# Performance work log

Measured on AMD Instinct MI355X. Metric: run time of the kernel, lower is better.

Reference implementation:

```python
import jax, jax.numpy as jnp
import numpy as np

D_MODEL = 1024
N_HEADS = 16
HEAD_DIM = D_MODEL // N_HEADS


def setup_inputs() -> dict:
    key = jax.random.key(0)
    k1, k2, k3 = jax.random.split(key, 3)
    x = jax.random.normal(k1, (4, 2048, D_MODEL), dtype=jnp.float32)
    # torch Linear(d, 3d, bias=False): y = x @ W.T with W [3d, d]; store transposed [d, 3d]
    s = 1.0 / np.sqrt(D_MODEL)
    w_qkv = jax.random.uniform(k2, (D_MODEL, 3 * D_MODEL), dtype=jnp.float32, minval=-s, maxval=s)
    w_proj = jax.random.uniform(k3, (D_MODEL, D_MODEL), dtype=jnp.float32, minval=-s, maxval=s)
    return {"x": x, "w_qkv": w_qkv, "w_proj": w_proj}


def reference(x, w_qkv, w_proj):
    B, T, D = x.shape
    qkv = (x @ w_qkv).reshape(B, T, 3, N_HEADS, HEAD_DIM)
    qkv = jnp.transpose(qkv, (2, 0, 3, 1, 4))  # [3, B, H, T, hd]
    q, k, v = qkv[0], qkv[1], qkv[2]
    # NOTE: original module applies NO 1/sqrt(head_dim) scaling
    attn = jax.nn.softmax(jnp.einsum('bhqd,bhkd->bhqk', q, k), axis=-1)
    out = jnp.einsum('bhqk,bhkd->bhqd', attn, v)
    out = jnp.transpose(out, (0, 2, 1, 3)).reshape(B, T, D)
    return out @ w_proj
```

## Files before the change

### kernel.cpp

```cpp
#include <hip/hip_runtime.h>

typedef __bf16 bf16;
typedef __bf16 bf16x8 __attribute__((ext_vector_type(8)));
typedef float f32x4 __attribute__((ext_vector_type(4)));
typedef unsigned int uint;
typedef unsigned short ushort;

typedef const __attribute__((address_space(1))) void* gas_ptr;
typedef __attribute__((address_space(3))) void* las_ptr;

__device__ __forceinline__ void load16_lds(const void* g, void* l) {
  __builtin_amdgcn_global_load_lds((gas_ptr)g, (las_ptr)l, 16, 0, 0);
}

__global__ __launch_bounds__(256) void cast_f32_bf16(
    const float* __restrict__ in, bf16* __restrict__ out) {
  size_t i = (size_t)blockIdx.x * 256 + threadIdx.x;
  const float4* p = reinterpret_cast<const float4*>(in) + i * 2;
  float4 a = p[0], b = p[1];
  bf16x8 v;
  v[0] = (bf16)a.x; v[1] = (bf16)a.y; v[2] = (bf16)a.z; v[3] = (bf16)a.w;
  v[4] = (bf16)b.x; v[5] = (bf16)b.y; v[6] = (bf16)b.z; v[7] = (bf16)b.w;
  reinterpret_cast<bf16x8*>(out)[i] = v;
}

__global__ __launch_bounds__(256) void transpose_f32_bf16(
    const float* __restrict__ in, bf16* __restrict__ out, int K, int N) {
  __shared__ __attribute__((aligned(16))) bf16 tile[64 * 72];
  const int k0 = blockIdx.y * 64, n0 = blockIdx.x * 64;
  const int tid = threadIdx.x;
  for (int c = tid; c < 1024; c += 256) {
    int ki = c >> 4, j4 = c & 15;
    float4 f = *reinterpret_cast<const float4*>(in + (size_t)(k0 + ki) * N + n0 + j4 * 4);
    bf16* t = &tile[ki * 72 + j4 * 4];
    t[0] = (bf16)f.x; t[1] = (bf16)f.y; t[2] = (bf16)f.z; t[3] = (bf16)f.w;
  }
  __syncthreads();
  for (int c = tid; c < 512; c += 256) {
    int ni = c >> 3, k8 = c & 7;
    bf16x8 v;
    for (int j = 0; j < 8; j++) v[j] = tile[(k8 * 8 + j) * 72 + ni];
    *reinterpret_cast<bf16x8*>(out + (size_t)(n0 + ni) * K + k0 + k8 * 8) = v;
  }
}

template <typename CT>
__global__ __launch_bounds__(256, 2) void gemm_lds(
    const bf16* __restrict__ A, const bf16* __restrict__ Bt,
    CT* __restrict__ C, int M, int N, int K) {
  __shared__ __attribute__((aligned(16))) bf16 As[128 * 64];
  __shared__ __attribute__((aligned(16))) bf16 Bs[128 * 64];
  const int tid = threadIdx.x;
  const int wave = tid >> 6;
  const int lane = tid & 63;
  const int l15 = lane & 15;
  const int quad = lane >> 4;
  const int nwg = gridDim.x * gridDim.y;
  const int orig = blockIdx.y * gridDim.x + blockIdx.x;
  const int swz = (orig & 7) * (nwg >> 3) + (orig >> 3);
  const int m0 = (swz / gridDim.x) * 128;
  const int n0 = (swz % gridDim.x) * 128;
  const int wm = (wave >> 1) * 64;
  const int wn = (wave & 1) * 64;

  f32x4 acc[4][4] = {};

  for (int kt = 0; kt < K; kt += 64) {
    __syncthreads();
    for (int it = 0; it < 4; ++it) {
      int p = it * 256 + wave * 64 + lane;
      int row = p >> 3, kc = (p & 7) ^ (row & 7);
      load16_lds(A + (size_t)(m0 + row) * K + kt + kc * 8, &As[p * 8]);
      load16_lds(Bt + (size_t)(n0 + row) * K + kt + kc * 8, &Bs[p * 8]);
    }
    __syncthreads();
    for (int kk = 0; kk < 64; kk += 32) {
      const int kc = (kk >> 3) + quad;
      bf16x8 af[4], bfr[4];
      for (int i = 0; i < 4; i++) {
        int row = wm + i * 16 + l15;
        af[i] = *reinterpret_cast<const bf16x8*>(&As[(row * 8 + (kc ^ (row & 7))) * 8]);
      }
      for (int j = 0; j < 4; j++) {
        int row = wn + j * 16 + l15;
        bfr[j] = *reinterpret_cast<const bf16x8*>(&Bs[(row * 8 + (kc ^ (row & 7))) * 8]);
      }
      for (int i = 0; i < 4; i++)
        for (int j = 0; j < 4; j++)
          acc[i][j] = __builtin_amdgcn_mfma_f32_16x16x32_bf16(af[i], bfr[j], acc[i][j], 0, 0, 0);
    }
  }

  for (int i = 0; i < 4; i++)
    for (int j = 0; j < 4; j++)
      for (int r = 0; r < 4; r++) {
        int row = m0 + wm + i * 16 + quad * 4 + r;
        int col = n0 + wn + j * 16 + l15;
        C[(size_t)row * N + col] = (CT)acc[i][j][r];
      }
}

__device__ __forceinline__ int vs_dw(int d, int kdw) {
  return d * 32 + (kdw ^ ((((d >> 3) ^ d) & 7) * 4));
}

__global__ __launch_bounds__(512, 4) void attn_kernel(
    const bf16* __restrict__ qkv, bf16* __restrict__ out) {
  __shared__ __attribute__((aligned(16))) bf16 Ks[2][64 * 64];
  __shared__ __attribute__((aligned(16))) uint Vs[2][64 * 32];

  const int tid = threadIdx.x;
  const int wave = tid >> 6;
  const int lane = tid & 63;
  const int l15 = lane & 15;
  const int quad = lane >> 4;
  const int b = blockIdx.x >> 4;
  const int h = blockIdx.x & 15;
  const int qt0 = blockIdx.y * 128;
  const bf16* base = qkv + (size_t)b * 2048 * 3072 + h * 64;
  const float L2E = 1.44269504f;

  bf16x8 aq0, aq1;
  {
    const bf16* qrow = base + (size_t)(qt0 + wave * 16 + l15) * 3072;
    aq0 = *reinterpret_cast<const bf16x8*>(qrow + quad * 8);
    aq1 = *reinterpret_cast<const bf16x8*>(qrow + 32 + quad * 8);
    for (int j = 0; j < 8; j++) {
      aq0[j] = (bf16)((float)aq0[j] * L2E);
      aq1[j] = (bf16)((float)aq1[j] * L2E);
    }
  }

  bf16x8 bones = {};
  if (l15 == 0)
    for (int j = 0; j < 8; j++) bones[j] = (bf16)1.0f;

  f32x4 nm = {};
  f32x4 o[4] = {};
  f32x4 l_acc = {};

  const int t2 = tid & 255;
  const int kp = t2 >> 3;
  const int oct = t2 & 7;
  const bool vrole = (wave < 4);
  const int prow = ((kp & 4) << 2) | ((kp & 24) >> 1) | (kp & 3);
  const int kxor = oct ^ (prow & 7);
  const int kdst0 = (prow * 8 + kxor) * 8;
  const int kdst1 = kdst0 + 32 * 64;

  bf16x8 pre0, pre1;
  if (vrole) {
    const bf16* v0p = base + (size_t)(2 * kp) * 3072 + 2048 + oct * 8;
    pre0 = *reinterpret_cast<const bf16x8*>(v0p);
    pre1 = *reinterpret_cast<const bf16x8*>(v0p + 3072);
  } else {
    const bf16* kb = base + 1024 + (size_t)kp * 3072 + oct * 8;
    pre0 = *reinterpret_cast<const bf16x8*>(kb);
    pre1 = *reinterpret_cast<const bf16x8*>(kb + (size_t)32 * 3072);
  }

  for (int kt = 0; kt < 2048; kt += 64) {
    const int cur = (kt >> 6) & 1;
    if (vrole) {
      const ushort* u0 = reinterpret_cast<const ushort*>(&pre0);
      const ushort* u1 = reinterpret_cast<const ushort*>(&pre1);
      for (int i = 0; i < 8; i++)
        Vs[cur][vs_dw(oct * 8 + i, kp)] = (uint)u0[i] | ((uint)u1[i] << 16);
    } else {
      *reinterpret_cast<bf16x8*>(&Ks[cur][kdst0]) = pre0;
      *reinterpret_cast<bf16x8*>(&Ks[cur][kdst1]) = pre1;
    }
    __syncthreads();

    if (kt + 64 < 2048) {
      const bf16* nb = base + (size_t)(kt + 64) * 3072;
      if (vrole) {
        const bf16* v0p = nb + (size_t)(2 * kp) * 3072 + 2048 + oct * 8;
        pre0 = *reinterpret_cast<const bf16x8*>(v0p);
        pre1 = *reinterpret_cast<const bf16x8*>(v0p + 3072);
      } else {
        const bf16* kb = nb + 1024 + (size_t)kp * 3072 + oct * 8;
        pre0 = *reinterpret_cast<const bf16x8*>(kb);
        pre1 = *reinterpret_cast<const bf16x8*>(kb + (size_t)32 * 3072);
      }
    }

    f32x4 s[4];
    __builtin_amdgcn_s_setprio(1);
    for (int n = 0; n < 4; n++) {
      int row = n * 16 + l15;
      int xr = row & 7;
      bf16x8 ak0 = *reinterpret_cast<const bf16x8*>(&Ks[cur][(row * 8 + (quad ^ xr)) * 8]);
      bf16x8 ak1 = *reinterpret_cast<const bf16x8*>(&Ks[cur][(row * 8 + ((4 + quad) ^ xr)) * 8]);
      f32x4 z = __builtin_amdgcn_mfma_f32_16x16x32_bf16(ak0, aq0, nm, 0, 0, 0);
      z = __builtin_amdgcn_mfma_f32_16x16x32_bf16(ak1, aq1, z, 0, 0, 0);
      s[n] = z;
    }
    __builtin_amdgcn_s_setprio(0);

    float mt = fmaxf(fmaxf(s[0][0], s[0][1]), s[0][2]);
    mt = fmaxf(fmaxf(mt, s[0][3]), s[1][0]);
    mt = fmaxf(fmaxf(mt, s[1][1]), s[1][2]);
    mt = fmaxf(fmaxf(mt, s[1][3]), s[2][0]);
    mt = fmaxf(fmaxf(mt, s[2][1]), s[2][2]);
    mt = fmaxf(fmaxf(mt, s[2][3]), s[3][0]);
    mt = fmaxf(fmaxf(mt, s[3][1]), s[3][2]);
    mt = fmaxf(mt, s[3][3]);

    if (!__all(mt <= 8.0f)) {
      mt = fmaxf(mt, __shfl_xor(mt, 16, 64));
      mt = fmaxf(mt, __shfl_xor(mt, 32, 64));
      mt = fmaxf(mt, 0.0f);
      float alpha = __builtin_amdgcn_exp2f(-mt);
      float v = nm[0] - mt;
      nm[0] = v; nm[1] = v; nm[2] = v; nm[3] = v;
      float a0 = __shfl(alpha, quad * 4 + 0, 64);
      float a1 = __shfl(alpha, quad * 4 + 1, 64);
      float a2 = __shfl(alpha, quad * 4 + 2, 64);
      float a3 = __shfl(alpha, quad * 4 + 3, 64);
      l_acc[0] *= a0; l_acc[1] *= a1; l_acc[2] *= a2; l_acc[3] *= a3;
      for (int n = 0; n < 4; n++) {
        o[n][0] *= a0; o[n][1] *= a1; o[n][2] *= a2; o[n][3] *= a3;
      }
      for (int n = 0; n < 4; n++)
        for (int r = 0; r < 4; r++) s[n][r] -= mt;
    }

    bf16x8 ap0, ap1;
    for (int r = 0; r < 4; r++) {
      ap0[r]     = (bf16)__builtin_amdgcn_exp2f(s[0][r]);
      ap0[4 + r] = (bf16)__builtin_amdgcn_exp2f(s[1][r]);
      ap1[r]     = (bf16)__builtin_amdgcn_exp2f(s[2][r]);
      ap1[4 + r] = (bf16)__builtin_amdgcn_exp2f(s[3][r]);
    }

    __builtin_amdgcn_s_setprio(1);
    l_acc = __builtin_amdgcn_mfma_f32_16x16x32_bf16(ap0, bones, l_acc, 0, 0, 0);
    l_acc = __builtin_amdgcn_mfma_f32_16x16x32_bf16(ap1, bones, l_acc, 0, 0, 0);

    for (int n = 0; n < 4; n++) {
      int d = n * 16 + l15;
      uint4 u0 = *reinterpret_cast<const uint4*>(&Vs[cur][vs_dw(d, quad * 4)]);
      uint4 u1 = *reinterpret_cast<const uint4*>(&Vs[cur][vs_dw(d, 16 + quad * 4)]);
      bf16x8 bv0 = *reinterpret_cast<const bf16x8*>(&u0);
      bf16x8 bv1 = *reinterpret_cast<const bf16x8*>(&u1);
      o[n] = __builtin_amdgcn_mfma_f32_16x16x32_bf16(ap0, bv0, o[n], 0, 0, 0);
      o[n] = __builtin_amdgcn_mfma_f32_16x16x32_bf16(ap1, bv1, o[n], 0, 0, 0);
    }
    __builtin_amdgcn_s_setprio(0);
  }

  for (int r = 0; r < 4; r++) {
    float lv = __shfl(l_acc[r], quad * 16, 64);
    float inv = 1.0f / lv;
    int q = qt0 + wave * 16 + quad * 4 + r;
    bf16* orow = out + (size_t)(b * 2048 + q) * 1024 + h * 64;
    for (int n = 0; n < 4; n++) orow[n * 16 + l15] = (bf16)(o[n][r] * inv);
  }
}

extern "C" void kernel_launch(void* const* d_in, const int* in_sizes, int n_in,
                              void* d_out, int out_size, void* d_ws, size_t ws_size,
                              hipStream_t stream) {
  const float* x = (const float*)d_in[0];
  const float* w_qkv = (const float*)d_in[1];
  const float* w_proj = (const float*)d_in[2];
  float* out = (float*)d_out;

  bf16* ws = (bf16*)d_ws;
  bf16* x_bf = ws;
  bf16* wqkvT = x_bf + (size_t)8192 * 1024;
  bf16* wprojT = wqkvT + 3072 * 1024;
  bf16* qkv = wprojT + 1024 * 1024;
  bf16* attn_out = qkv + (size_t)8192 * 3072;

  cast_f32_bf16<<<4096, 256, 0, stream>>>(x, x_bf);
  transpose_f32_bf16<<<dim3(48, 16), 256, 0, stream>>>(w_qkv, wqkvT, 1024, 3072);
  transpose_f32_bf16<<<dim3(16, 16), 256, 0, stream>>>(w_proj, wprojT, 1024, 1024);
  gemm_lds<bf16><<<dim3(24, 64), 256, 0, stream>>>(x_bf, wqkvT, qkv, 8192, 3072, 1024);
  attn_kernel<<<dim3(64, 16), 512, 0, stream>>>(qkv, attn_out);
  gemm_lds<float><<<dim3(8, 64), 256, 0, stream>>>(attn_out, wprojT, out, 8192, 1024, 1024);
}
```

Baseline: 269.7 us.

## Load K tiles directly to LDS and split V staging across all waves

```diff
diff --git a/kernel.cpp b/kernel.cpp
--- a/kernel.cpp
+++ b/kernel.cpp
@@ -2,6 +2,7 @@
 
 typedef __bf16 bf16;
 typedef __bf16 bf16x8 __attribute__((ext_vector_type(8)));
+typedef __bf16 bf16x4 __attribute__((ext_vector_type(4)));
 typedef float f32x4 __attribute__((ext_vector_type(4)));
 typedef unsigned int uint;
 typedef unsigned short ushort;
@@ -139,50 +140,36 @@
   f32x4 o[4] = {};
   f32x4 l_acc = {};
 
-  const int t2 = tid & 255;
-  const int kp = t2 >> 3;
-  const int oct = t2 & 7;
-  const bool vrole = (wave < 4);
-  const int prow = ((kp & 4) << 2) | ((kp & 24) >> 1) | (kp & 3);
-  const int kxor = oct ^ (prow & 7);
-  const int kdst0 = (prow * 8 + kxor) * 8;
-  const int kdst1 = kdst0 + 32 * 64;
-
-  bf16x8 pre0, pre1;
-  if (vrole) {
-    const bf16* v0p = base + (size_t)(2 * kp) * 3072 + 2048 + oct * 8;
-    pre0 = *reinterpret_cast<const bf16x8*>(v0p);
-    pre1 = *reinterpret_cast<const bf16x8*>(v0p + 3072);
-  } else {
-    const bf16* kb = base + 1024 + (size_t)kp * 3072 + oct * 8;
-    pre0 = *reinterpret_cast<const bf16x8*>(kb);
-    pre1 = *reinterpret_cast<const bf16x8*>(kb + (size_t)32 * 3072);
-  }
+  const int c = tid;
+  const int krow = c >> 3;
+  const int kc8 = (c & 7) ^ (krow & 7);
+  const int ktrue = (((krow >> 4) & 1) << 2) | (((krow >> 3) & 1) << 4) |
+                    (((krow >> 2) & 1) << 3) | (krow & 3) | (krow & 32);
+  const bf16* kgp = base + 1024 + (size_t)ktrue * 3072 + kc8 * 8;
+
+  const int vkp = tid >> 4;
+  const int vd0 = (tid & 15) * 4;
+  const bf16* vgp = base + (size_t)(2 * vkp) * 3072 + 2048 + vd0;
+
+  load16_lds(kgp, &Ks[0][c * 8]);
+  bf16x4 vpre0 = *reinterpret_cast<const bf16x4*>(vgp);
+  bf16x4 vpre1 = *reinterpret_cast<const bf16x4*>(vgp + 3072);
 
   for (int kt = 0; kt < 2048; kt += 64) {
     const int cur = (kt >> 6) & 1;
-    if (vrole) {
-      const ushort* u0 = reinterpret_cast<const ushort*>(&pre0);
-      const ushort* u1 = reinterpret_cast<const ushort*>(&pre1);
-      for (int i = 0; i < 8; i++)
-        Vs[cur][vs_dw(oct * 8 + i, kp)] = (uint)u0[i] | ((uint)u1[i] << 16);
-    } else {
-      *reinterpret_cast<bf16x8*>(&Ks[cur][kdst0]) = pre0;
-      *reinterpret_cast<bf16x8*>(&Ks[cur][kdst1]) = pre1;
+    {
+      const ushort* u0 = reinterpret_cast<const ushort*>(&vpre0);
+      const ushort* u1 = reinterpret_cast<const ushort*>(&vpre1);
+      for (int i = 0; i < 4; i++)
+        Vs[cur][vs_dw(vd0 + i, vkp)] = (uint)u0[i] | ((uint)u1[i] << 16);
     }
     __syncthreads();
 
     if (kt + 64 < 2048) {
-      const bf16* nb = base + (size_t)(kt + 64) * 3072;
-      if (vrole) {
-        const bf16* v0p = nb + (size_t)(2 * kp) * 3072 + 2048 + oct * 8;
-        pre0 = *reinterpret_cast<const bf16x8*>(v0p);
-        pre1 = *reinterpret_cast<const bf16x8*>(v0p + 3072);
-      } else {
-        const bf16* kb = nb + 1024 + (size_t)kp * 3072 + oct * 8;
-        pre0 = *reinterpret_cast<const bf16x8*>(kb);
-        pre1 = *reinterpret_cast<const bf16x8*>(kb + (size_t)32 * 3072);
-      }
+      const size_t off = (size_t)(kt + 64) * 3072;
+      load16_lds(kgp + off, &Ks[cur ^ 1][c * 8]);
+      vpre0 = *reinterpret_cast<const bf16x4*>(vgp + off);
+      vpre1 = *reinterpret_cast<const bf16x4*>(vgp + off + 3072);
     }
 
     f32x4 s[4];
```

Result: slower. 277.6 us (+2.9%).
